# Optimization experiments

Hardware: AMD Instinct MI355X
Metric: run time of the kernel (lower is better)

## Reference

```python
import jax, jax.numpy as jnp
import numpy as np

N = 100000      # nodes
E = 3200000     # edges
F_IN = 1433     # Cora num_node_features
H = 16          # hidden channels
C = 7           # Cora num_classes


def setup_inputs() -> dict:
    key = jax.random.key(0)
    ks = jax.random.split(key, 8)
    x = jax.random.normal(ks[0], (N, F_IN), dtype=jnp.float32)
    edge_index = jax.random.randint(ks[1], (2, E), 0, N, dtype=jnp.int64)
    W1 = jax.random.normal(ks[2], (F_IN, H), dtype=jnp.float32) * (1.0 / np.sqrt(F_IN))
    b1 = jnp.zeros((H,), dtype=jnp.float32)
    W2 = jax.random.normal(ks[3], (H, H), dtype=jnp.float32) * (1.0 / np.sqrt(H))
    b2 = jnp.zeros((H,), dtype=jnp.float32)
    W3 = jax.random.normal(ks[4], (H, C), dtype=jnp.float32) * (1.0 / np.sqrt(H))
    b3 = jnp.zeros((C,), dtype=jnp.float32)
    return {"x": x, "W1": W1, "b1": b1, "W2": W2, "b2": b2,
            "W3": W3, "b3": b3, "edge_index": edge_index}


def reference(x, W1, b1, W2, b2, W3, b3, edge_index):
    # Add self loops (GCNConv default) and compute symmetric normalization once;
    # it is identical for all three layers.
    loop = jnp.arange(N, dtype=edge_index.dtype)
    src = jnp.concatenate([edge_index[0], loop])
    dst = jnp.concatenate([edge_index[1], loop])
    deg = jax.ops.segment_sum(jnp.ones_like(dst, dtype=x.dtype), dst, num_segments=N)
    dinv = jnp.where(deg > 0, jax.lax.rsqrt(deg), 0.0)
    norm = dinv[src] * dinv[dst]  # [E+N]

    def conv(h, W, b):
        h = h @ W                                   # [N, out]
        msg = h[src] * norm[:, None]                # gather + scale, [E+N, out]
        return jax.ops.segment_sum(msg, dst, num_segments=N) + b

    h = jax.nn.relu(conv(x, W1, b1))
    h = jax.nn.relu(conv(h, W2, b2))
    logits = conv(h, W3, b3)
    return jax.nn.log_softmax(logits, axis=1)
```

## Files before the change

kernel.cpp:

```cpp
#include <hip/hip_runtime.h>
#include <hip/hip_fp16.h>

#define F_IN 1433
#define BCAP 96
#define KSTR 1480


typedef _Float16 f16x8 __attribute__((ext_vector_type(8)));
typedef float    f32x4 __attribute__((ext_vector_type(4)));

__global__ __launch_bounds__(256) void k_zero(int* __restrict__ p, int n) {
    int i = blockIdx.x * 256 + threadIdx.x;
    if (i < n) p[i] = 0;
}

__global__ __launch_bounds__(256) void k_scatter(const int* __restrict__ ei,
    int* cnt, int* bucket, int E, int N)
{
    int e = blockIdx.x * 256 + threadIdx.x;
    if (e < E) {
        int s = ei[e], d = ei[E + e];
        if ((unsigned)s < (unsigned)N && (unsigned)d < (unsigned)N) {
            int slot = atomicAdd(&cnt[d], 1);
            if (slot < BCAP) bucket[(size_t)d * BCAP + slot] = s;
        }
    }
}

__global__ __launch_bounds__(256) void k_gemm(
    const float* __restrict__ x, const float* __restrict__ W1,
    const int* __restrict__ cnt, float* __restrict__ s, int N)
{
    __shared__ _Float16 wt[16 * KSTR];
    int tid = threadIdx.x;
    for (int i = tid; i < 16 * 1472; i += 256) {
        int c = i & 15, k = i >> 4;
        float v = (k < F_IN) ? W1[k * 16 + c] : 0.0f;
        wt[c * KSTR + k] = (_Float16)v;
    }
    __syncthreads();

    int wv = tid >> 6, lane = tid & 63;
    int npairs = (N + 31) >> 5;
    int pair = blockIdx.x * 4 + wv;
    if (pair >= npairs) return;

    int rc = lane & 15;
    int g  = lane >> 4;
    int rowA = pair * 32 + rc;
    int rowB = rowA + 16;
    const float* xr0 = x + (size_t)((rowA < N) ? rowA : (N - 1)) * F_IN;
    const float* xr1 = x + (size_t)((rowB < N) ? rowB : (N - 1)) * F_IN;
    const _Float16* wrow = wt + rc * KSTR;

    struct __attribute__((packed, aligned(4))) f4u { float f[4]; };

    f32x4 acc0 = {0.0f, 0.0f, 0.0f, 0.0f};
    f32x4 acc1 = {0.0f, 0.0f, 0.0f, 0.0f};
    int kb = g * 8;

    #pragma unroll 2
    for (int ch = 0; ch < 44; ++ch) {
        int k0 = ch * 32 + kb;
        f4u xa0 = *(const f4u*)&xr0[k0];
        f4u xb0 = *(const f4u*)&xr0[k0 + 4];
        f4u xa1 = *(const f4u*)&xr1[k0];
        f4u xb1 = *(const f4u*)&xr1[k0 + 4];
        f16x8 bv = *(const f16x8*)&wrow[k0];
        f16x8 av0, av1;
        #pragma unroll
        for (int j = 0; j < 4; ++j) {
            av0[j]     = (_Float16)xa0.f[j];
            av0[j + 4] = (_Float16)xb0.f[j];
            av1[j]     = (_Float16)xa1.f[j];
            av1[j + 4] = (_Float16)xb1.f[j];
        }
        acc0 = __builtin_amdgcn_mfma_f32_16x16x32_f16(av0, bv, acc0, 0, 0, 0);
        acc1 = __builtin_amdgcn_mfma_f32_16x16x32_f16(av1, bv, acc1, 0, 0, 0);
    }
    {
        int k0 = 1408 + kb;
        f16x8 av0, av1, bv;
        bv = *(const f16x8*)&wrow[k0];
        #pragma unroll
        for (int j = 0; j < 8; ++j) {
            int k = k0 + j;
            bool ok = k < F_IN;
            av0[j] = (_Float16)(ok ? xr0[k] : 0.0f);
            av1[j] = (_Float16)(ok ? xr1[k] : 0.0f);
        }
        acc0 = __builtin_amdgcn_mfma_f32_16x16x32_f16(av0, bv, acc0, 0, 0, 0);
        acc1 = __builtin_amdgcn_mfma_f32_16x16x32_f16(av1, bv, acc1, 0, 0, 0);
    }

    #pragma unroll
    for (int r = 0; r < 4; ++r) {
        int growA = pair * 32 + g * 4 + r;
        int growB = growA + 16;
        if (growA < N) {
            float di = rsqrtf((float)cnt[growA] + 1.0f);
            s[growA * 16 + rc] = acc0[r] * di;
        }
        if (growB < N) {
            float di = rsqrtf((float)cnt[growB] + 1.0f);
            s[growB * 16 + rc] = acc1[r] * di;
        }
    }
}

__global__ __launch_bounds__(256) void k_aggA(
    const int* __restrict__ cnt, const int* __restrict__ bucket,
    const float* __restrict__ sin, const float* __restrict__ W,
    const float* __restrict__ bias, float* __restrict__ sout, int N)
{
    __shared__ float w[256], bs[16];
    int tid = threadIdx.x;
    w[tid] = W[tid];
    if (tid < 16) bs[tid] = bias[tid];
    __syncthreads();

    int wave = tid >> 6, lane = tid & 63;
    int dst = blockIdx.x * 4 + wave;
    if (dst >= N) return;
    int g = lane >> 4, c = lane & 15;
    int deg = min(cnt[dst], BCAP);
    const int* bk = bucket + (size_t)dst * BCAP;

    int e0 = (lane < deg)      ? bk[lane]      : 0;
    int e1 = (64 + lane < deg) ? bk[64 + lane] : 0;

    float acc = (g == 0) ? sin[dst * 16 + c] : 0.0f;
    for (int base = 0; base < deg; base += 32) {
        float vs = 0.0f;
        #pragma unroll
        for (int i = 0; i < 8; ++i) {
            int j = base + g + 4 * i;
            int sa = __shfl(e0, j & 63, 64), sb = __shfl(e1, j & 63, 64);
            int sv = (j < 64) ? sa : sb;
            float v = (j < deg) ? sin[sv * 16 + c] : 0.0f;
            vs += v;
        }
        acc += vs;
    }
    acc += __shfl_xor(acc, 16, 64);
    acc += __shfl_xor(acc, 32, 64);

    float di = rsqrtf((float)cnt[dst] + 1.0f);
    float h = fmaxf(fmaf(di, acc, bs[c]), 0.0f);
    float t = 0.0f;
    #pragma unroll
    for (int k = 0; k < 16; ++k)
        t = fmaf(__shfl(h, k, 16), w[k * 16 + c], t);
    if (lane < 16) sout[dst * 16 + c] = di * t;
}

__global__ __launch_bounds__(256) void k_aggB(
    const int* __restrict__ cnt, const int* __restrict__ bucket,
    const float* __restrict__ sin, const float* __restrict__ W,
    const float* __restrict__ bias, float* __restrict__ sout, int N)
{
    __shared__ float w[112], bs[16];
    int tid = threadIdx.x;
    if (tid < 112) w[tid] = W[tid];
    if (tid < 16) bs[tid] = bias[tid];
    __syncthreads();

    int wave = tid >> 6, lane = tid & 63;
    int dst = blockIdx.x * 4 + wave;
    if (dst >= N) return;
    int g = lane >> 4, c = lane & 15;
    int deg = min(cnt[dst], BCAP);
    const int* bk = bucket + (size_t)dst * BCAP;

    int e0 = (lane < deg)      ? bk[lane]      : 0;
    int e1 = (64 + lane < deg) ? bk[64 + lane] : 0;

    float acc = (g == 0) ? sin[dst * 16 + c] : 0.0f;
    for (int base = 0; base < deg; base += 32) {
        float vs = 0.0f;
        #pragma unroll
        for (int i = 0; i < 8; ++i) {
            int j = base + g + 4 * i;
            int sa = __shfl(e0, j & 63, 64), sb = __shfl(e1, j & 63, 64);
            int sv = (j < 64) ? sa : sb;
            float v = (j < deg) ? sin[sv * 16 + c] : 0.0f;
            vs += v;
        }
        acc += vs;
    }
    acc += __shfl_xor(acc, 16, 64);
    acc += __shfl_xor(acc, 32, 64);

    float di = rsqrtf((float)cnt[dst] + 1.0f);
    float h = fmaxf(fmaf(di, acc, bs[c]), 0.0f);
    int cc = (c < 7) ? c : 0;
    float t = 0.0f;
    #pragma unroll
    for (int k = 0; k < 16; ++k)
        t = fmaf(__shfl(h, k, 16), w[k * 7 + cc], t);
    if (lane < 7) sout[dst * 7 + c] = di * t;
}

__global__ __launch_bounds__(256) void k_aggC(
    const int* __restrict__ cnt, const int* __restrict__ bucket,
    const float* __restrict__ sin, const float* __restrict__ bias,
    float* __restrict__ out, int N)
{
    __shared__ float bs[8];
    int tid = threadIdx.x;
    if (tid < 7) bs[tid] = bias[tid];
    if (tid == 7) bs[7] = 0.0f;
    __syncthreads();

    int wave = tid >> 6, lane = tid & 63;
    int dst = blockIdx.x * 4 + wave;
    if (dst >= N) return;
    int g8 = lane >> 3, c8 = lane & 7;
    bool c7 = (c8 < 7);
    int cc = c7 ? c8 : 0;
    int deg = min(cnt[dst], BCAP);
    const int* bk = bucket + (size_t)dst * BCAP;

    int e0 = (lane < deg)      ? bk[lane]      : 0;
    int e1 = (64 + lane < deg) ? bk[64 + lane] : 0;

    float acc = (g8 == 0 && c7) ? sin[dst * 7 + c8] : 0.0f;
    for (int base = 0; base < deg; base += 64) {
        float vs = 0.0f;
        #pragma unroll
        for (int i = 0; i < 8; ++i) {
            int j = base + g8 + 8 * i;
            int sa = __shfl(e0, j & 63, 64), sb = __shfl(e1, j & 63, 64);
            int sv = (j < 64) ? sa : sb;
            float v = (j < deg && c7) ? sin[sv * 7 + cc] : 0.0f;
            vs += v;
        }
        acc += vs;
    }
    acc += __shfl_xor(acc, 8, 64);
    acc += __shfl_xor(acc, 16, 64);
    acc += __shfl_xor(acc, 32, 64);

    if (lane < 8) {
        float di = rsqrtf((float)cnt[dst] + 1.0f);
        float logit = c7 ? fmaf(di, acc, bs[c8]) : -1e30f;
        float m = logit;
        m = fmaxf(m, __shfl_xor(m, 1, 8));
        m = fmaxf(m, __shfl_xor(m, 2, 8));
        m = fmaxf(m, __shfl_xor(m, 4, 8));
        float e = c7 ? expf(logit - m) : 0.0f;
        float ssum = e;
        ssum += __shfl_xor(ssum, 1, 8);
        ssum += __shfl_xor(ssum, 2, 8);
        ssum += __shfl_xor(ssum, 4, 8);
        if (c7) out[dst * 7 + c8] = logit - m - logf(ssum);
    }
}

extern "C" void kernel_launch(void* const* d_in, const int* in_sizes, int n_in,
                              void* d_out, int out_size, void* d_ws, size_t ws_size,
                              hipStream_t stream)
{
    const float* x  = (const float*)d_in[0];
    const float* W1 = (const float*)d_in[1];
    const float* b1 = (const float*)d_in[2];
    const float* W2 = (const float*)d_in[3];
    const float* b2 = (const float*)d_in[4];
    const float* W3 = (const float*)d_in[5];
    const float* b3 = (const float*)d_in[6];
    const int*   ei = (const int*)d_in[7];
    float* out = (float*)d_out;

    int N = in_sizes[0] / F_IN;
    int E = in_sizes[7] / 2;

    int*   cnt    = (int*)d_ws;
    int*   bucket = cnt + N;
    float* s1     = (float*)(bucket + (size_t)N * BCAP);
    float* s2     = s1 + 16 * (size_t)N;
    float* s3     = s2 + 16 * (size_t)N;

    int nbN = (N + 255) / 256;
    int nbE = (E + 255) / 256;
    int nb4 = (N + 3) / 4;
    int npairs = (N + 31) / 32;
    int nbG = (npairs + 3) / 4;

    k_zero   <<<nbN, 256, 0, stream>>>(cnt, N);
    k_scatter<<<nbE, 256, 0, stream>>>(ei, cnt, bucket, E, N);
    k_gemm   <<<nbG, 256, 0, stream>>>(x, W1, cnt, s1, N);
    k_aggA   <<<nb4, 256, 0, stream>>>(cnt, bucket, s1, W2, b1, s2, N);
    k_aggB   <<<nb4, 256, 0, stream>>>(cnt, bucket, s2, W3, b2, s3, N);
    k_aggC   <<<nb4, 256, 0, stream>>>(cnt, bucket, s3, b3, out, N);
}
```

Baseline: 571.5 us.

## Precompute fp16 W1 once in global memory and use one 16-row tile per wave

The fp16 transpose of W1 moves out of every GEMM block's shared memory into a global buffer, filled once by a prep kernel that also zeroes the degree counts. The GEMM no longer uses about 47KB of LDS per block and no longer rebuilds W per block. Each wave now handles one 16-row tile instead of two, with launch bounds of 4 blocks per CU and a deeper unroll. This should raise occupancy and drop the per-block W setup, but W reads now come from global or cache instead of LDS, and each wave has less independent work to hide latency.

```diff
diff --git a/kernel.cpp b/kernel.cpp
--- a/kernel.cpp
+++ b/kernel.cpp
@@ -3,15 +3,22 @@
 
 #define F_IN 1433
 #define BCAP 96
-#define KSTR 1480
+#define WSTR 2048
 
 
 typedef _Float16 f16x8 __attribute__((ext_vector_type(8)));
 typedef float    f32x4 __attribute__((ext_vector_type(4)));
 
-__global__ __launch_bounds__(256) void k_zero(int* __restrict__ p, int n) {
+__global__ __launch_bounds__(256) void k_prep(const float* __restrict__ W1,
+    int* __restrict__ cnt, _Float16* __restrict__ wt, int N)
+{
     int i = blockIdx.x * 256 + threadIdx.x;
-    if (i < n) p[i] = 0;
+    if (i < N) cnt[i] = 0;
+    if (i < 16 * WSTR) {
+        int c = i >> 11, k = i & (WSTR - 1);
+        float v = (k < F_IN) ? W1[k * 16 + c] : 0.0f;
+        wt[i] = (_Float16)v;
+    }
 }
 
 __global__ __launch_bounds__(256) void k_scatter(const int* __restrict__ ei,
@@ -27,83 +34,59 @@
     }
 }
 
-__global__ __launch_bounds__(256) void k_gemm(
-    const float* __restrict__ x, const float* __restrict__ W1,
+__global__ __launch_bounds__(256, 4) void k_gemm(
+    const float* __restrict__ x, const _Float16* __restrict__ wt,
     const int* __restrict__ cnt, float* __restrict__ s, int N)
 {
-    __shared__ _Float16 wt[16 * KSTR];
-    int tid = threadIdx.x;
-    for (int i = tid; i < 16 * 1472; i += 256) {
-        int c = i & 15, k = i >> 4;
-        float v = (k < F_IN) ? W1[k * 16 + c] : 0.0f;
-        wt[c * KSTR + k] = (_Float16)v;
-    }
-    __syncthreads();
-
+    int tid = threadIdx.x;
     int wv = tid >> 6, lane = tid & 63;
-    int npairs = (N + 31) >> 5;
-    int pair = blockIdx.x * 4 + wv;
-    if (pair >= npairs) return;
+    int ntiles = (N + 15) >> 4;
+    int tile = blockIdx.x * 4 + wv;
+    if (tile >= ntiles) return;
 
     int rc = lane & 15;
     int g  = lane >> 4;
-    int rowA = pair * 32 + rc;
-    int rowB = rowA + 16;
-    const float* xr0 = x + (size_t)((rowA < N) ? rowA : (N - 1)) * F_IN;
-    const float* xr1 = x + (size_t)((rowB < N) ? rowB : (N - 1)) * F_IN;
-    const _Float16* wrow = wt + rc * KSTR;
+    int row = tile * 16 + rc;
+    const float* xr = x + (size_t)((row < N) ? row : (N - 1)) * F_IN;
+    const _Float16* wrow = wt + (rc << 11);
 
     struct __attribute__((packed, aligned(4))) f4u { float f[4]; };
 
-    f32x4 acc0 = {0.0f, 0.0f, 0.0f, 0.0f};
-    f32x4 acc1 = {0.0f, 0.0f, 0.0f, 0.0f};
+    f32x4 acc = {0.0f, 0.0f, 0.0f, 0.0f};
     int kb = g * 8;
 
-    #pragma unroll 2
+    #pragma unroll 4
     for (int ch = 0; ch < 44; ++ch) {
         int k0 = ch * 32 + kb;
-        f4u xa0 = *(const f4u*)&xr0[k0];
-        f4u xb0 = *(const f4u*)&xr0[k0 + 4];
-        f4u xa1 = *(const f4u*)&xr1[k0];
-        f4u xb1 = *(const f4u*)&xr1[k0 + 4];
+        f4u xa = *(const f4u*)&xr[k0];
+        f4u xb = *(const f4u*)&xr[k0 + 4];
         f16x8 bv = *(const f16x8*)&wrow[k0];
-        f16x8 av0, av1;
+        f16x8 av;
         #pragma unroll
         for (int j = 0; j < 4; ++j) {
-            av0[j]     = (_Float16)xa0.f[j];
-            av0[j + 4] = (_Float16)xb0.f[j];
-            av1[j]     = (_Float16)xa1.f[j];
-            av1[j + 4] = (_Float16)xb1.f[j];
-        }
-        acc0 = __builtin_amdgcn_mfma_f32_16x16x32_f16(av0, bv, acc0, 0, 0, 0);
-        acc1 = __builtin_amdgcn_mfma_f32_16x16x32_f16(av1, bv, acc1, 0, 0, 0);
+            av[j]     = (_Float16)xa.f[j];
+            av[j + 4] = (_Float16)xb.f[j];
+        }
+        acc = __builtin_amdgcn_mfma_f32_16x16x32_f16(av, bv, acc, 0, 0, 0);
     }
     {
         int k0 = 1408 + kb;
-        f16x8 av0, av1, bv;
+        f16x8 av, bv;
         bv = *(const f16x8*)&wrow[k0];
         #pragma unroll
         for (int j = 0; j < 8; ++j) {
             int k = k0 + j;
-            bool ok = k < F_IN;
-            av0[j] = (_Float16)(ok ? xr0[k] : 0.0f);
-            av1[j] = (_Float16)(ok ? xr1[k] : 0.0f);
-        }
-        acc0 = __builtin_amdgcn_mfma_f32_16x16x32_f16(av0, bv, acc0, 0, 0, 0);
-        acc1 = __builtin_amdgcn_mfma_f32_16x16x32_f16(av1, bv, acc1, 0, 0, 0);
+            av[j] = (_Float16)((k < F_IN) ? xr[k] : 0.0f);
+        }
+        acc = __builtin_amdgcn_mfma_f32_16x16x32_f16(av, bv, acc, 0, 0, 0);
     }
 
     #pragma unroll
     for (int r = 0; r < 4; ++r) {
-        int growA = pair * 32 + g * 4 + r;
-        int growB = growA + 16;
-        if (growA < N) {
-            float di = rsqrtf((float)cnt[growA] + 1.0f);
-            s[growA * 16 + rc] = acc0[r] * di;
-        }
-        if (growB < N) {
-            float di = rsqrtf((float)cnt[growB] + 1.0f);
-            s[growB * 16 + rc] = acc1[r] * di;
+        int grow = tile * 16 + g * 4 + r;
+        if (grow < N) {
+            float di = rsqrtf((float)cnt[grow] + 1.0f);
+            s[grow * 16 + rc] = acc[r] * di;
         }
     }
 }
@@ -274,21 +257,22 @@
     int N = in_sizes[0] / F_IN;
     int E = in_sizes[7] / 2;
 
-    int*   cnt    = (int*)d_ws;
-    int*   bucket = cnt + N;
-    float* s1     = (float*)(bucket + (size_t)N * BCAP);
-    float* s2     = s1 + 16 * (size_t)N;
-    float* s3     = s2 + 16 * (size_t)N;
+    int*      cnt    = (int*)d_ws;
+    int*      bucket = cnt + N;
+    _Float16* wt     = (_Float16*)(bucket + (size_t)N * BCAP);
+    float*    s1     = (float*)(wt + 16 * WSTR);
+    float*    s2     = s1 + 16 * (size_t)N;
+    float*    s3     = s2 + 16 * (size_t)N;
 
     int nbN = (N + 255) / 256;
     int nbE = (E + 255) / 256;
     int nb4 = (N + 3) / 4;
-    int npairs = (N + 31) / 32;
-    int nbG = (npairs + 3) / 4;
-
-    k_zero   <<<nbN, 256, 0, stream>>>(cnt, N);
+    int ntiles = (N + 15) / 16;
+    int nbG = (ntiles + 3) / 4;
+
+    k_prep   <<<nbN, 256, 0, stream>>>(W1, cnt, wt, N);
     k_scatter<<<nbE, 256, 0, stream>>>(ei, cnt, bucket, E, N);
-    k_gemm   <<<nbG, 256, 0, stream>>>(x, W1, cnt, s1, N);
+    k_gemm   <<<nbG, 256, 0, stream>>>(x, wt, cnt, s1, N);
     k_aggA   <<<nb4, 256, 0, stream>>>(cnt, bucket, s1, W2, b1, s2, N);
     k_aggB   <<<nb4, 256, 0, stream>>>(cnt, bucket, s2, W3, b2, s3, N);
     k_aggC   <<<nb4, 256, 0, stream>>>(cnt, bucket, s3, b3, out, N);
```

Measured after the change: 504.2 us. 1.13x faster.
